# Performance work log

Measured on AMD Instinct MI355X. Metric: run time of the kernel, lower is better.

## Reference

```python
import jax, jax.numpy as jnp
import numpy as np

B, T, HIDDEN, QLR = 1, 2560, 7168, 1536
N_HEADS, HEAD_DIM, ROPE_DIM, TOPK = 64, 128, 64, 2048
LN_EPS = 1e-6


def _rope(x, cos, sin):
    # non-interleaved (half-split) rotary: pairs are (x[i], x[i+d/2])
    d = x.shape[-1] // 2
    x1, x2 = x[..., :d], x[..., d:]
    return jnp.concatenate([x1 * cos - x2 * sin, x1 * sin + x2 * cos], axis=-1)


def setup_inputs() -> dict:
    key = jax.random.key(0)
    ks = jax.random.split(key, 6)
    x = jax.random.normal(ks[0], (B, T, HIDDEN), dtype=jnp.float32)
    qr = jax.random.normal(ks[1], (B, T, QLR), dtype=jnp.float32)
    # rope tables (theta = 10000)
    inv_freq = 1.0 / (10000.0 ** (jnp.arange(0, ROPE_DIM, 2, dtype=jnp.float32) / ROPE_DIM))
    angles = jnp.arange(T, dtype=jnp.float32)[:, None] * inv_freq[None, :]  # [T, 32]
    freqs_cos = jnp.cos(angles)
    freqs_sin = jnp.sin(angles)
    # causal additive mask
    i = jnp.arange(T)
    mask = jnp.where(i[None, :, None] >= i[None, None, :], 0.0, -1e9).astype(jnp.float32)  # [1,T,T]
    # params (torch Linear stored transposed so y = x @ W)
    s = 0.02
    wq_b = jax.random.normal(ks[2], (QLR, N_HEADS * HEAD_DIM), dtype=jnp.float32) * s
    wk_w = jax.random.normal(ks[3], (HIDDEN, HEAD_DIM), dtype=jnp.float32) * s
    k_gamma = jnp.ones((HEAD_DIM,), dtype=jnp.float32)
    k_beta = jnp.zeros((HEAD_DIM,), dtype=jnp.float32)
    wproj = jax.random.normal(ks[4], (HIDDEN, N_HEADS), dtype=jnp.float32) * s
    return {"x": x, "qr": qr, "freqs_cos": freqs_cos, "freqs_sin": freqs_sin,
            "mask": mask, "wq_b": wq_b, "wk_w": wk_w, "k_gamma": k_gamma,
            "k_beta": k_beta, "wproj": wproj}


def reference(x, qr, freqs_cos, freqs_sin, mask, wq_b, wk_w, k_gamma, k_beta, wproj):
    bsz, seqlen, _ = x.shape
    # queries
    q = (qr @ wq_b).reshape(bsz, seqlen, N_HEADS, HEAD_DIM)
    q_pe, q_nope = q[..., :ROPE_DIM], q[..., ROPE_DIM:]
    q_pe = _rope(q_pe, freqs_cos[None, :, None, :], freqs_sin[None, :, None, :])
    q = jnp.concatenate([q_pe, q_nope], axis=-1)  # [B,T,H,D]
    # keys: layernorm(wk(x))
    k = x @ wk_w  # [B,T,D]
    mu = jnp.mean(k, axis=-1, keepdims=True)
    var = jnp.mean(jnp.square(k - mu), axis=-1, keepdims=True)
    k = (k - mu) / jnp.sqrt(var + LN_EPS) * k_gamma + k_beta
    k_pe, k_nope = k[..., :ROPE_DIM], k[..., ROPE_DIM:]
    k_pe = _rope(k_pe, freqs_cos[None, :, :], freqs_sin[None, :, :])
    k = jnp.concatenate([k_pe, k_nope], axis=-1)  # [B,S,D]
    # per-head weights
    weights = (x @ wproj) * (N_HEADS ** -0.5) * (HEAD_DIM ** -0.5)  # [B,T,H]
    # relu score + weighted head reduce
    logits = jax.nn.relu(jnp.einsum('bthd,bsd->btsh', q, k))  # [B,T,S,H]
    index_score = jnp.einsum('btsh,bth->bts', logits, weights) + mask
    # top-k + scatter mask
    kk = min(TOPK, seqlen)
    _, topk_idx = jax.lax.top_k(index_score, kk)  # [B,T,K]
    index_mask = jnp.full((bsz, seqlen, seqlen), -1e9, dtype=jnp.float32)
    bi = jnp.arange(bsz)[:, None, None]
    ti = jnp.arange(seqlen)[None, :, None]
    index_mask = index_mask.at[bi, ti, topk_idx].set(0.0)
    return index_mask
```

## Files before the change

kernel.cpp:

```cpp
#include <hip/hip_runtime.h>
#include <cstdint>

#define T_SEQ   2560
#define HID     7168
#define QLRD    1536
#define NHEAD   64
#define HDIM    128
#define TOPK    2048
#define T0SEL   2048
#define NSEL    512

#define QHOFF 0
#define QLOFF 2097152
#define KOFF  4194304
#define WOFF  4521984
#define KHOFF 4554752
#define KLOFF 4718592
#define SOFF  5242880

typedef _Float16 half8 __attribute__((ext_vector_type(8)));
typedef _Float16 half4v __attribute__((ext_vector_type(4)));
typedef float    floatx16 __attribute__((ext_vector_type(16)));

__global__ __launch_bounds__(384) void kw_kernel(
        const float* __restrict__ x, const float* __restrict__ wk,
        const float* __restrict__ wp, float* __restrict__ Pk,
        float* __restrict__ Pw, long pkstride, long pwstride, int klen) {
    const int t0 = blockIdx.x * 64;
    const int chunk = blockIdx.y;
    const int k0 = chunk * klen;
    const int kl = min(klen, HID - k0);
    const int steps = kl >> 5;
    float* pk = Pk + (size_t)chunk * pkstride;
    float* pw = Pw + (size_t)chunk * pwstride;

    const int tid = threadIdx.x;
    const int lane = tid & 63;
    const int wv = tid >> 6;
    const int wt = wv / 3;
    const int wn2 = wv % 3;
    const int l31 = lane & 31;
    const int kb = (lane >> 5) * 8;

    __shared__ __align__(16) _Float16 Ah[64 * 40];
    __shared__ __align__(16) _Float16 Al[64 * 40];
    __shared__ __align__(16) _Float16 Bh[192 * 40];
    __shared__ __align__(16) _Float16 Bl[192 * 40];

    const int am = tid >> 2;
    const int ak = (tid & 3) * 8;
    const int bkr = (tid / 48) * 4;
    const int bnr = (tid % 48) * 4;

    const float* aptr = x + (size_t)(t0 + am) * HID + k0 + ak;
    const float* bsrc; int bld, bcol;
    if (bnr < 128) { bsrc = wk; bld = 128; bcol = bnr; }
    else           { bsrc = wp; bld = 64;  bcol = bnr - 128; }
    const float* bptr = bsrc + (size_t)(k0 + bkr) * bld + bcol;

    float4 pa0, pa1;
    if (tid < 256) { pa0 = *(const float4*)(aptr + 0); pa1 = *(const float4*)(aptr + 4); }
    float4 pb0 = *(const float4*)(bptr + 0 * (size_t)bld);
    float4 pb1 = *(const float4*)(bptr + 1 * (size_t)bld);
    float4 pb2 = *(const float4*)(bptr + 2 * (size_t)bld);
    float4 pb3 = *(const float4*)(bptr + 3 * (size_t)bld);

    floatx16 Z = {0.f,0.f,0.f,0.f,0.f,0.f,0.f,0.f,0.f,0.f,0.f,0.f,0.f,0.f,0.f,0.f};
    floatx16 Chh0 = Z, Chl0 = Z, Clh0 = Z;
    floatx16 Chh1 = Z, Chl1 = Z, Clh1 = Z;

    for (int ks = 0; ks < steps; ++ks) {
        __syncthreads();
        if (tid < 256) {
            float av[8];
            *(float4*)&av[0] = pa0; *(float4*)&av[4] = pa1;
            half8 ha, la;
#pragma unroll
            for (int i = 0; i < 8; ++i) {
                float v = av[i];
                _Float16 hi = (_Float16)v;
                ha[i] = hi;
                la[i] = (_Float16)(v - (float)hi);
            }
            *(half8*)&Ah[am * 40 + ak] = ha;
            *(half8*)&Al[am * 40 + ak] = la;
        }
        {
            float bv[4][4];
            *(float4*)&bv[0][0] = pb0; *(float4*)&bv[1][0] = pb1;
            *(float4*)&bv[2][0] = pb2; *(float4*)&bv[3][0] = pb3;
#pragma unroll
            for (int j = 0; j < 4; ++j) {
                half4v hb, lb;
#pragma unroll
                for (int i = 0; i < 4; ++i) {
                    float v = bv[i][j] * 64.0f;
                    _Float16 hi = (_Float16)v;
                    hb[i] = hi;
                    lb[i] = (_Float16)(v - (float)hi);
                }
                *(half4v*)&Bh[(bnr + j) * 40 + bkr] = hb;
                *(half4v*)&Bl[(bnr + j) * 40 + bkr] = lb;
            }
        }
        __syncthreads();
        if (ks + 1 < steps) {
            aptr += 32; bptr += (size_t)32 * bld;
            if (tid < 256) { pa0 = *(const float4*)(aptr + 0); pa1 = *(const float4*)(aptr + 4); }
            pb0 = *(const float4*)(bptr + 0 * (size_t)bld);
            pb1 = *(const float4*)(bptr + 1 * (size_t)bld);
            pb2 = *(const float4*)(bptr + 2 * (size_t)bld);
            pb3 = *(const float4*)(bptr + 3 * (size_t)bld);
        }
#pragma unroll
        for (int c = 0; c < 2; ++c) {
            const int ka = c * 16 + kb;
            half8 ah  = *(const half8*)&Ah[(wt * 32 + l31) * 40 + ka];
            half8 al  = *(const half8*)&Al[(wt * 32 + l31) * 40 + ka];
            half8 bh0 = *(const half8*)&Bh[(wn2 * 64 + l31) * 40 + ka];
            half8 bl0 = *(const half8*)&Bl[(wn2 * 64 + l31) * 40 + ka];
            half8 bh1 = *(const half8*)&Bh[(wn2 * 64 + 32 + l31) * 40 + ka];
            half8 bl1 = *(const half8*)&Bl[(wn2 * 64 + 32 + l31) * 40 + ka];
            Chh0 = __builtin_amdgcn_mfma_f32_32x32x16_f16(ah, bh0, Chh0, 0, 0, 0);
            Chl0 = __builtin_amdgcn_mfma_f32_32x32x16_f16(ah, bl0, Chl0, 0, 0, 0);
            Clh0 = __builtin_amdgcn_mfma_f32_32x32x16_f16(al, bh0, Clh0, 0, 0, 0);
            Chh1 = __builtin_amdgcn_mfma_f32_32x32x16_f16(ah, bh1, Chh1, 0, 0, 0);
            Chl1 = __builtin_amdgcn_mfma_f32_32x32x16_f16(ah, bl1, Chl1, 0, 0, 0);
            Clh1 = __builtin_amdgcn_mfma_f32_32x32x16_f16(al, bh1, Clh1, 0, 0, 0);
        }
    }

    const int rbase = wt * 32 + 4 * (lane >> 5);
#pragma unroll
    for (int r = 0; r < 16; ++r) {
        int trow = t0 + rbase + (r & 3) + 8 * (r >> 2);
        float v0 = ((Chh0[r] + Chl0[r]) + Clh0[r]) * 0.015625f;
        float v1 = ((Chh1[r] + Chl1[r]) + Clh1[r]) * 0.015625f;
        int c0 = wn2 * 64 + l31;
        if (wn2 < 2) {
            pk[(size_t)trow * 128 + c0] = v0;
            pk[(size_t)trow * 128 + c0 + 32] = v1;
        } else if (trow >= T0SEL) {
            pw[(size_t)(trow - T0SEL) * 64 + c0 - 128] = v0;
            pw[(size_t)(trow - T0SEL) * 64 + c0 - 96] = v1;
        }
    }
}

__global__ void reduce2_kernel(float* __restrict__ dk, const float* __restrict__ sk,
                               long kstr, float* __restrict__ dw,
                               const float* __restrict__ sw, long wstr, int nchunk) {
    int i = blockIdx.x * 256 + threadIdx.x;
    if (i < 327680) {
        float s = sk[i];
        for (int c = 1; c < nchunk; ++c) s += sk[(size_t)c * kstr + i];
        dk[i] = s;
    } else {
        int j = i - 327680;
        float s = sw[j];
        for (int c = 1; c < nchunk; ++c) s += sw[(size_t)c * wstr + j];
        dw[j] = s;
    }
}

__global__ void lnrope_kernel(const float* __restrict__ fcos, const float* __restrict__ fsin,
                              const float* __restrict__ gamma, const float* __restrict__ beta,
                              const float* __restrict__ Kbuf, float* __restrict__ Wbuf,
                              _Float16* __restrict__ KhG, _Float16* __restrict__ KlG) {
#pragma clang fp contract(off)
    const int s = blockIdx.x;
    const int d = threadIdx.x;
    __shared__ float red[128];
    __shared__ float kn[128];
    float kv = Kbuf[(size_t)s * 128 + d];
    red[d] = kv;
    __syncthreads();
    for (int off = 64; off > 0; off >>= 1) {
        if (d < off) red[d] += red[d + off];
        __syncthreads();
    }
    float mu = red[0] / 128.0f;
    __syncthreads();
    float dv = kv - mu;
    red[d] = dv * dv;
    __syncthreads();
    for (int off = 64; off > 0; off >>= 1) {
        if (d < off) red[d] += red[d + off];
        __syncthreads();
    }
    float var = red[0] / 128.0f;
    float nrm = dv / sqrtf(var + 1e-6f);
    nrm = nrm * gamma[d] + beta[d];
    kn[d] = nrm;
    __syncthreads();
    float o;
    if (d < 64) {
        int p = d & 31;
        float c = fcos[s * 32 + p], sn = fsin[s * 32 + p];
        if (d < 32) o = kn[d] * c - kn[d + 32] * sn;
        else        o = kn[d - 32] * sn + kn[d] * c;
    } else {
        o = kn[d];
    }
    _Float16 hi = (_Float16)o;
    _Float16 lo = (_Float16)(o - (float)hi);
    KhG[(size_t)s * 128 + d] = hi;
    KlG[(size_t)s * 128 + d] = lo;
    if (s >= T0SEL && d < 64) {
        Wbuf[(size_t)(s - T0SEL) * 64 + d] *= (0.125f * 0.08838834764831845f);
    }
}

__global__ __launch_bounds__(256, 3) void q_kernel(
        const float* __restrict__ qr, const float* __restrict__ wqb,
        const float* __restrict__ fcos, const float* __restrict__ fsin,
        _Float16* __restrict__ QhG, _Float16* __restrict__ QlG) {
    const int bx = blockIdx.x;
    const int head = blockIdx.y;
    const int tid = threadIdx.x;
    const int lane = tid & 63;
    const int wv = tid >> 6;
    const int wt = wv >> 1, wn = wv & 1;
    const int l31 = lane & 31;
    const int kb = (lane >> 5) * 8;

    __shared__ __align__(16) _Float16 Ah[64 * 40];
    __shared__ __align__(16) _Float16 Al[64 * 40];
    __shared__ __align__(16) _Float16 Bh[128 * 40];
    __shared__ __align__(16) _Float16 Bl[128 * 40];

    const int am = tid >> 2;
    const int ak = (tid & 3) * 8;
    const int bn = (tid & 31) * 4;
    const int bk = (tid >> 5) * 4;

    const float* aptr = qr + (size_t)(T0SEL + bx * 64 + am) * QLRD + ak;
    const float* bptr = wqb + (size_t)bk * 8192 + head * 128 + bn;

    float4 pa0 = *(const float4*)(aptr + 0);
    float4 pa1 = *(const float4*)(aptr + 4);
    float4 pb0 = *(const float4*)(bptr + 0 * 8192);
    float4 pb1 = *(const float4*)(bptr + 1 * 8192);
    float4 pb2 = *(const float4*)(bptr + 2 * 8192);
    float4 pb3 = *(const float4*)(bptr + 3 * 8192);

    floatx16 Z = {0.f,0.f,0.f,0.f,0.f,0.f,0.f,0.f,0.f,0.f,0.f,0.f,0.f,0.f,0.f,0.f};
    floatx16 Chh0 = Z, Chl0 = Z, Clh0 = Z;
    floatx16 Chh1 = Z, Chl1 = Z, Clh1 = Z;

    for (int ks = 0; ks < QLRD / 32; ++ks) {
        __syncthreads();
        {
            float av[8];
            *(float4*)&av[0] = pa0; *(float4*)&av[4] = pa1;
            half8 ha, la;
#pragma unroll
            for (int i = 0; i < 8; ++i) {
                float v = av[i];
                _Float16 hi = (_Float16)v;
                ha[i] = hi;
                la[i] = (_Float16)(v - (float)hi);
            }
            *(half8*)&Ah[am * 40 + ak] = ha;
            *(half8*)&Al[am * 40 + ak] = la;
        }
        {
            float bv[4][4];
            *(float4*)&bv[0][0] = pb0; *(float4*)&bv[1][0] = pb1;
            *(float4*)&bv[2][0] = pb2; *(float4*)&bv[3][0] = pb3;
#pragma unroll
            for (int j = 0; j < 4; ++j) {
                half4v hb, lb;
#pragma unroll
                for (int i = 0; i < 4; ++i) {
                    float v = bv[i][j] * 64.0f;
                    _Float16 hi = (_Float16)v;
                    hb[i] = hi;
                    lb[i] = (_Float16)(v - (float)hi);
                }
                *(half4v*)&Bh[(bn + j) * 40 + bk] = hb;
                *(half4v*)&Bl[(bn + j) * 40 + bk] = lb;
            }
        }
        __syncthreads();
        if (ks + 1 < QLRD / 32) {
            aptr += 32; bptr += (size_t)32 * 8192;
            pa0 = *(const float4*)(aptr + 0);
            pa1 = *(const float4*)(aptr + 4);
            pb0 = *(const float4*)(bptr + 0 * 8192);
            pb1 = *(const float4*)(bptr + 1 * 8192);
            pb2 = *(const float4*)(bptr + 2 * 8192);
            pb3 = *(const float4*)(bptr + 3 * 8192);
        }
#pragma unroll
        for (int c = 0; c < 2; ++c) {
            const int ka = c * 16 + kb;
            half8 ah = *(const half8*)&Ah[(wt * 32 + l31) * 40 + ka];
            half8 al = *(const half8*)&Al[(wt * 32 + l31) * 40 + ka];
            half8 bh0 = *(const half8*)&Bh[(wn * 64 + l31) * 40 + ka];
            half8 bl0 = *(const half8*)&Bl[(wn * 64 + l31) * 40 + ka];
            half8 bh1 = *(const half8*)&Bh[(wn * 64 + 32 + l31) * 40 + ka];
            half8 bl1 = *(const half8*)&Bl[(wn * 64 + 32 + l31) * 40 + ka];
            Chh0 = __builtin_amdgcn_mfma_f32_32x32x16_f16(ah, bh0, Chh0, 0, 0, 0);
            Chl0 = __builtin_amdgcn_mfma_f32_32x32x16_f16(ah, bl0, Chl0, 0, 0, 0);
            Clh0 = __builtin_amdgcn_mfma_f32_32x32x16_f16(al, bh0, Clh0, 0, 0, 0);
            Chh1 = __builtin_amdgcn_mfma_f32_32x32x16_f16(ah, bh1, Chh1, 0, 0, 0);
            Chl1 = __builtin_amdgcn_mfma_f32_32x32x16_f16(ah, bl1, Chl1, 0, 0, 0);
            Clh1 = __builtin_amdgcn_mfma_f32_32x32x16_f16(al, bh1, Clh1, 0, 0, 0);
        }
    }

    {
#pragma clang fp contract(off)
        const int tbase = bx * 64 + wt * 32 + 4 * (lane >> 5);
#pragma unroll
        for (int r = 0; r < 16; ++r) {
            int tl = tbase + (r & 3) + 8 * (r >> 2);
            float v0 = ((Chh0[r] + Chl0[r]) + Clh0[r]) * 0.015625f;
            float v1 = ((Chh1[r] + Chl1[r]) + Clh1[r]) * 0.015625f;
            float o0, o1;
            if (wn == 0) {
                int tg = T0SEL + tl;
                float c = fcos[tg * 32 + l31];
                float s = fsin[tg * 32 + l31];
                o0 = v0 * c - v1 * s;
                o1 = v0 * s + v1 * c;
            } else {
                o0 = v0; o1 = v1;
            }
            int d0 = wn * 64 + l31;
            size_t off = (size_t)head * 65536 + (size_t)tl * 128;
            _Float16 h0 = (_Float16)o0;
            _Float16 h1 = (_Float16)o1;
            QhG[off + d0] = h0;
            QlG[off + d0] = (_Float16)(o0 - (float)h0);
            QhG[off + d0 + 32] = h1;
            QlG[off + d0 + 32] = (_Float16)(o1 - (float)h1);
        }
    }
}

__global__ __launch_bounds__(256) void score_kernel(
        const _Float16* __restrict__ Qh, const _Float16* __restrict__ Ql,
        const _Float16* __restrict__ Kh, const _Float16* __restrict__ Kl,
        const float* __restrict__ Wbuf, float* __restrict__ S0,
        float* __restrict__ S1, int hcnt) {
    const int bid = blockIdx.x;
    const int tt0 = (bid & 15) * 32;
    const int s0  = (bid >> 4) * 128;
    const int hb  = blockIdx.y * hcnt;
    const int he  = hb + hcnt;
    float* __restrict__ dst = blockIdx.y ? S1 : S0;
    const int tid = threadIdx.x;
    const int wv  = tid >> 6;
    const int lane = tid & 63;
    const int l31 = lane & 31;
    const int kb  = (lane >> 5) * 8;

    __shared__ _Float16 Ah[2][32 * 136];
    __shared__ _Float16 Al[2][32 * 136];
    __shared__ float WsT[64 * 36];

    half8 Bh[8], Bl[8];
    {
        const int srow = s0 + wv * 32 + l31;
        const _Float16* kh = Kh + (size_t)srow * 128 + kb;
        const _Float16* kl = Kl + (size_t)srow * 128 + kb;
#pragma unroll
        for (int c = 0; c < 8; ++c) {
            Bh[c] = *(const half8*)(kh + c * 16);
            Bl[c] = *(const half8*)(kl + c * 16);
        }
    }
#pragma unroll
    for (int r = 0; r < 8; ++r) {
        int idx = tid + 256 * r;
        int row = idx >> 6, h = idx & 63;
        WsT[h * 36 + row] = Wbuf[(size_t)(tt0 + row) * 64 + h];
    }

    {
        const _Float16* qh = Qh + (size_t)hb * 65536 + (size_t)tt0 * 128;
        const _Float16* ql = Ql + (size_t)hb * 65536 + (size_t)tt0 * 128;
#pragma unroll
        for (int r = 0; r < 2; ++r) {
            int idx = tid + 256 * r;
            int row = idx >> 4, c = idx & 15;
            *(half8*)&Ah[0][row * 136 + c * 8] = *(const half8*)&qh[row * 128 + c * 8];
            *(half8*)&Al[0][row * 136 + c * 8] = *(const half8*)&ql[row * 128 + c * 8];
        }
    }

    float S[16];
#pragma unroll
    for (int r = 0; r < 16; ++r) S[r] = 0.0f;

    for (int h = hb; h < he; ++h) {
        __syncthreads();
        if (h + 1 < he) {
            const _Float16* qh = Qh + (size_t)(h + 1) * 65536 + (size_t)tt0 * 128;
            const _Float16* ql = Ql + (size_t)(h + 1) * 65536 + (size_t)tt0 * 128;
            _Float16* dh = Ah[(h + 1) & 1];
            _Float16* dl = Al[(h + 1) & 1];
#pragma unroll
            for (int r = 0; r < 2; ++r) {
                int idx = tid + 256 * r;
                int row = idx >> 4, c = idx & 15;
                *(half8*)&dh[row * 136 + c * 8] = *(const half8*)&qh[row * 128 + c * 8];
                *(half8*)&dl[row * 136 + c * 8] = *(const half8*)&ql[row * 128 + c * 8];
            }
        }
        const _Float16* ah_ = Ah[h & 1];
        const _Float16* al_ = Al[h & 1];

        floatx16 C0 = {0.f,0.f,0.f,0.f,0.f,0.f,0.f,0.f,0.f,0.f,0.f,0.f,0.f,0.f,0.f,0.f};
        floatx16 C1 = C0, C2 = C0, C3 = C0;
#pragma unroll
        for (int c = 0; c < 8; ++c) {
            half8 a_h = *(const half8*)&ah_[l31 * 136 + c * 16 + kb];
            half8 a_l = *(const half8*)&al_[l31 * 136 + c * 16 + kb];
            C0 = __builtin_amdgcn_mfma_f32_32x32x16_f16(a_h, Bh[c], C0, 0, 0, 0);
            C1 = __builtin_amdgcn_mfma_f32_32x32x16_f16(a_l, Bl[c], C1, 0, 0, 0);
            C2 = __builtin_amdgcn_mfma_f32_32x32x16_f16(a_h, Bl[c], C2, 0, 0, 0);
            C3 = __builtin_amdgcn_mfma_f32_32x32x16_f16(a_l, Bh[c], C3, 0, 0, 0);
        }
        const float* wb = &WsT[h * 36 + 4 * (lane >> 5)];
        float4 w0 = *(const float4*)(wb + 0);
        float4 w1 = *(const float4*)(wb + 8);
        float4 w2 = *(const float4*)(wb + 16);
        float4 w3 = *(const float4*)(wb + 24);
        float w[16] = {w0.x, w0.y, w0.z, w0.w, w1.x, w1.y, w1.z, w1.w,
                       w2.x, w2.y, w2.z, w2.w, w3.x, w3.y, w3.z, w3.w};
#pragma unroll
        for (int r = 0; r < 16; ++r) {
            float L = (C0[r] + C1[r]) + (C2[r] + C3[r]);
            S[r] += w[r] * fmaxf(L, 0.0f);
        }
    }
    const int scol = s0 + wv * 32 + l31;
#pragma unroll
    for (int r = 0; r < 16; ++r) {
        int trow = tt0 + (r & 3) + 8 * (r >> 2) + 4 * (lane >> 5);
        dst[(size_t)trow * 2560 + scol] = S[r] + 0.0f;
    }
}

__global__ void finalize_kernel(float* __restrict__ out, const float* __restrict__ S1) {
    const int row_id = blockIdx.x;
    const int tid = threadIdx.x;

    if (row_id < T0SEL) {
        const float4 zero4 = make_float4(0.0f, 0.0f, 0.0f, 0.0f);
        const float4 neg4 = make_float4(-1000000000.0f, -1000000000.0f,
                                        -1000000000.0f, -1000000000.0f);
        for (int i = tid; i < T_SEQ / 4; i += 256) {
            *(float4*)&out[(size_t)row_id * T_SEQ + i * 4] = (i * 4 < TOPK) ? zero4 : neg4;
        }
        return;
    }

    const int t = row_id;
    const int n = t + 1;
    float* row = out + (size_t)t * T_SEQ;
    const float* s1p = S1 ? (S1 + (size_t)(t - T0SEL) * T_SEQ) : nullptr;

    __shared__ unsigned U[T_SEQ];
    __shared__ int hist[256];
    __shared__ int aux[256];
    __shared__ unsigned sh_prefix;
    __shared__ int sh_kneed;

    for (int i = tid; i < T_SEQ; i += 256) {
        unsigned u = 0u;
        if (i < n) {
            float sc = row[i];
            if (s1p) sc += s1p[i];
            int b = __float_as_int(sc);
            u = (b < 0) ? ~((unsigned)b) : (((unsigned)b) | 0x80000000u);
        }
        U[i] = u;
    }
    if (tid == 0) { sh_prefix = 0u; sh_kneed = TOPK; }
    __syncthreads();

    for (int pass = 0; pass < 4; ++pass) {
        const int shift = 24 - 8 * pass;
        const unsigned himask = (pass == 0) ? 0u : (0xFFFFFFFFu << (shift + 8));
        hist[tid] = 0;
        __syncthreads();
        const unsigned pre = sh_prefix;
        const int kneed = sh_kneed;
        for (int i = tid; i < T_SEQ; i += 256) {
            unsigned u = U[i];
            if ((u & himask) == pre) atomicAdd(&hist[(u >> shift) & 255], 1);
        }
        __syncthreads();
        aux[tid] = hist[tid];
        __syncthreads();
        for (int off = 1; off < 256; off <<= 1) {
            int a = (tid + off < 256) ? aux[tid + off] : 0;
            __syncthreads();
            aux[tid] += a;
            __syncthreads();
        }
        int above = (tid < 255) ? aux[tid + 1] : 0;
        if (above < kneed && kneed <= aux[tid]) {
            sh_prefix = pre | (((unsigned)tid) << shift);
            sh_kneed = kneed - above;
        }
        __syncthreads();
    }
    const unsigned theta = sh_prefix;
    const int r = sh_kneed;

    const int s_lo = tid * 10, s_hi = s_lo + 10;
    int c = 0;
    for (int s = s_lo; s < s_hi; ++s) c += (U[s] == theta);
    aux[tid] = c;
    __syncthreads();
    for (int off = 1; off < 256; off <<= 1) {
        int a = (tid >= off) ? aux[tid - off] : 0;
        __syncthreads();
        aux[tid] += a;
        __syncthreads();
    }
    int rank = aux[tid] - c;
    for (int s = s_lo; s < s_hi; ++s) {
        unsigned u = U[s];
        bool sel = (u > theta) || (u == theta && rank < r);
        if (u == theta) ++rank;
        row[s] = sel ? 0.0f : -1000000000.0f;
    }
}

extern "C" void kernel_launch(void* const* d_in, const int* in_sizes, int n_in,
                              void* d_out, int out_size, void* d_ws, size_t ws_size,
                              hipStream_t stream) {
    (void)in_sizes; (void)n_in; (void)out_size;
    const float* x     = (const float*)d_in[0];
    const float* qr    = (const float*)d_in[1];
    const float* fcos  = (const float*)d_in[2];
    const float* fsin  = (const float*)d_in[3];
    const float* wqb   = (const float*)d_in[5];
    const float* wk    = (const float*)d_in[6];
    const float* gamma = (const float*)d_in[7];
    const float* beta  = (const float*)d_in[8];
    const float* wp    = (const float*)d_in[9];

    float* out  = (float*)d_out;
    float* Kbuf = out + KOFF;
    float* Wbuf = out + WOFF;
    float* Sbuf = out + SOFF;
    _Float16* QhG = (_Float16*)(out + QHOFF);
    _Float16* QlG = (_Float16*)(out + QLOFF);
    _Float16* KhG = (_Float16*)(out + KHOFF);
    _Float16* KlG = (_Float16*)(out + KLOFF);

    const size_t need = (size_t)(6 * 327680 + 6 * 32768) * 4;
    int nchunk; int klen; float *Pk, *Pw; long pkstride, pwstride;
    if (ws_size >= need) {
        nchunk = 6; klen = 1216;
        Pk = (float*)d_ws;            pkstride = 327680;
        Pw = (float*)d_ws + 1966080;  pwstride = 32768;
    } else {
        nchunk = 2; klen = 3584;
        Pk = out + KOFF;  pkstride = 360448;
        Pw = out + WOFF;  pwstride = 360448;
    }

    const size_t s1_need = (size_t)NSEL * T_SEQ * sizeof(float);
    float* S1 = (ws_size >= s1_need) ? (float*)d_ws : nullptr;

    kw_kernel<<<dim3(40, nchunk), 384, 0, stream>>>(x, wk, wp, Pk, Pw, pkstride, pwstride, klen);
    reduce2_kernel<<<1408, 256, 0, stream>>>(Kbuf, Pk, pkstride, Wbuf, Pw, pwstride, nchunk);
    lnrope_kernel<<<T_SEQ, 128, 0, stream>>>(fcos, fsin, gamma, beta, Kbuf, Wbuf, KhG, KlG);
    q_kernel<<<dim3(8, 64), 256, 0, stream>>>(qr, wqb, fcos, fsin, QhG, QlG);
    if (S1) {
        score_kernel<<<dim3(320, 2), 256, 0, stream>>>(QhG, QlG, KhG, KlG, Wbuf, Sbuf, S1, 32);
    } else {
        score_kernel<<<dim3(320, 1), 256, 0, stream>>>(QhG, QlG, KhG, KlG, Wbuf, Sbuf, nullptr, 64);
    }
    finalize_kernel<<<T_SEQ, 256, 0, stream>>>(out, S1);
}
```

Measured before the change: 427.5 us.

## Load Q fragments directly from global and drop low-low split-fp16 MFMA term

```diff
diff --git a/kernel.cpp b/kernel.cpp
--- a/kernel.cpp
+++ b/kernel.cpp
@@ -357,8 +357,6 @@
     const int l31 = lane & 31;
     const int kb  = (lane >> 5) * 8;
 
-    __shared__ _Float16 Ah[2][32 * 136];
-    __shared__ _Float16 Al[2][32 * 136];
     __shared__ float WsT[64 * 36];
 
     half8 Bh[8], Bl[8];
@@ -378,51 +376,31 @@
         int row = idx >> 6, h = idx & 63;
         WsT[h * 36 + row] = Wbuf[(size_t)(tt0 + row) * 64 + h];
     }
-
-    {
-        const _Float16* qh = Qh + (size_t)hb * 65536 + (size_t)tt0 * 128;
-        const _Float16* ql = Ql + (size_t)hb * 65536 + (size_t)tt0 * 128;
-#pragma unroll
-        for (int r = 0; r < 2; ++r) {
-            int idx = tid + 256 * r;
-            int row = idx >> 4, c = idx & 15;
-            *(half8*)&Ah[0][row * 136 + c * 8] = *(const half8*)&qh[row * 128 + c * 8];
-            *(half8*)&Al[0][row * 136 + c * 8] = *(const half8*)&ql[row * 128 + c * 8];
-        }
-    }
+    __syncthreads();
+
+    const _Float16* qhp = Qh + (size_t)hb * 65536 + (size_t)(tt0 + l31) * 128 + kb;
+    const _Float16* qlp = Ql + (size_t)hb * 65536 + (size_t)(tt0 + l31) * 128 + kb;
 
     float S[16];
 #pragma unroll
     for (int r = 0; r < 16; ++r) S[r] = 0.0f;
 
     for (int h = hb; h < he; ++h) {
-        __syncthreads();
-        if (h + 1 < he) {
-            const _Float16* qh = Qh + (size_t)(h + 1) * 65536 + (size_t)tt0 * 128;
-            const _Float16* ql = Ql + (size_t)(h + 1) * 65536 + (size_t)tt0 * 128;
-            _Float16* dh = Ah[(h + 1) & 1];
-            _Float16* dl = Al[(h + 1) & 1];
-#pragma unroll
-            for (int r = 0; r < 2; ++r) {
-                int idx = tid + 256 * r;
-                int row = idx >> 4, c = idx & 15;
-                *(half8*)&dh[row * 136 + c * 8] = *(const half8*)&qh[row * 128 + c * 8];
-                *(half8*)&dl[row * 136 + c * 8] = *(const half8*)&ql[row * 128 + c * 8];
-            }
-        }
-        const _Float16* ah_ = Ah[h & 1];
-        const _Float16* al_ = Al[h & 1];
+        half8 a_h[8], a_l[8];
+#pragma unroll
+        for (int c = 0; c < 8; ++c) {
+            a_h[c] = *(const half8*)(qhp + c * 16);
+            a_l[c] = *(const half8*)(qlp + c * 16);
+        }
+        qhp += 65536; qlp += 65536;
 
         floatx16 C0 = {0.f,0.f,0.f,0.f,0.f,0.f,0.f,0.f,0.f,0.f,0.f,0.f,0.f,0.f,0.f,0.f};
-        floatx16 C1 = C0, C2 = C0, C3 = C0;
+        floatx16 C2 = C0, C3 = C0;
 #pragma unroll
         for (int c = 0; c < 8; ++c) {
-            half8 a_h = *(const half8*)&ah_[l31 * 136 + c * 16 + kb];
-            half8 a_l = *(const half8*)&al_[l31 * 136 + c * 16 + kb];
-            C0 = __builtin_amdgcn_mfma_f32_32x32x16_f16(a_h, Bh[c], C0, 0, 0, 0);
-            C1 = __builtin_amdgcn_mfma_f32_32x32x16_f16(a_l, Bl[c], C1, 0, 0, 0);
-            C2 = __builtin_amdgcn_mfma_f32_32x32x16_f16(a_h, Bl[c], C2, 0, 0, 0);
-            C3 = __builtin_amdgcn_mfma_f32_32x32x16_f16(a_l, Bh[c], C3, 0, 0, 0);
+            C0 = __builtin_amdgcn_mfma_f32_32x32x16_f16(a_h[c], Bh[c], C0, 0, 0, 0);
+            C2 = __builtin_amdgcn_mfma_f32_32x32x16_f16(a_h[c], Bl[c], C2, 0, 0, 0);
+            C3 = __builtin_amdgcn_mfma_f32_32x32x16_f16(a_l[c], Bh[c], C3, 0, 0, 0);
         }
         const float* wb = &WsT[h * 36 + 4 * (lane >> 5)];
         float4 w0 = *(const float4*)(wb + 0);
@@ -433,7 +411,7 @@
                        w2.x, w2.y, w2.z, w2.w, w3.x, w3.y, w3.z, w3.w};
 #pragma unroll
         for (int r = 0; r < 16; ++r) {
-            float L = (C0[r] + C1[r]) + (C2[r] + C3[r]);
+            float L = (C0[r] + C2[r]) + C3[r];
             S[r] += w[r] * fmaxf(L, 0.0f);
         }
     }
```

Measured after the change: 510.9 us. 19.5% more time.
